# Kernel tuning notes

Measured on AMD Instinct MI355X. Metric: run time of the kernel, lower is better.

Reference implementation:

```python
import jax, jax.numpy as jnp
import numpy as np

D_MODEL = 96
D_STATE = 16
D_INNER = 192   # expand * d_model
DT_RANK = 6     # ceil(96/16)
D_DEPTH_OUT = 1024  # (64/2)*(64/2)
BATCH, HH, WW = 2, 64, 64


def silu(v):
    return v * jax.nn.sigmoid(v)


def setup_inputs() -> dict:
    key = jax.random.key(0)
    ks = jax.random.split(key, 10)
    f = jnp.float32
    x = jax.random.normal(ks[0], (BATCH, HH, WW, D_MODEL), f)
    in_proj_w = jax.random.normal(ks[1], (2 * D_INNER, D_MODEL), f) * 0.02
    conv2d_w = jax.random.normal(ks[2], (D_INNER, 1, 3, 3), f) * 0.1  # depthwise, groups=D_INNER
    conv2d_b = jnp.zeros((D_INNER,), f)
    depth_conv_w = jax.random.normal(ks[3], (D_INNER, 1, 3, 3), f) * 0.1  # depthwise, stride 2
    depth_conv_b = jnp.zeros((D_INNER,), f)
    depth_fc_w = jax.random.normal(ks[4], (D_INNER, D_DEPTH_OUT), f) * 0.02
    depth_fc_b = jnp.zeros((D_INNER,), f)
    x_proj_w = jax.random.normal(ks[5], (DT_RANK + 2 * D_STATE, D_INNER), f) * 0.02
    dt_init_std = DT_RANK ** (-0.5)
    dt_projs_w = jax.random.uniform(ks[6], (D_INNER, DT_RANK), f, -dt_init_std, dt_init_std)
    # inverse-softplus of dt ~ U(log 1e-3, log 0.1)
    dt = jnp.exp(jax.random.uniform(ks[7], (D_INNER,), f) * (np.log(0.1) - np.log(0.001)) + np.log(0.001))
    dt = jnp.clip(dt, 1e-4, None)
    dt_projs_b = dt + jnp.log(-jnp.expm1(-dt))
    A_logs = jnp.log(jnp.tile(jnp.arange(1, D_STATE + 1, dtype=f)[None, :], (D_INNER, 1)))
    Ds = jnp.ones((D_INNER,), f)
    out_norm_w = jnp.ones((D_INNER,), f)
    out_norm_b = jnp.zeros((D_INNER,), f)
    out_proj_w = jax.random.normal(ks[8], (D_MODEL, D_INNER), f) * 0.02
    return dict(x=x, in_proj_w=in_proj_w, conv2d_w=conv2d_w, conv2d_b=conv2d_b,
                depth_conv_w=depth_conv_w, depth_conv_b=depth_conv_b,
                depth_fc_w=depth_fc_w, depth_fc_b=depth_fc_b, x_proj_w=x_proj_w,
                dt_projs_w=dt_projs_w, dt_projs_b=dt_projs_b, A_logs=A_logs, Ds=Ds,
                out_norm_w=out_norm_w, out_norm_b=out_norm_b, out_proj_w=out_proj_w)


def _selective_scan(u, delta, A, Bm, Cm, D, delta_bias):
    # u, delta: [B, D, L]; A: [D, N]; Bm, Cm: [B, N, L]; D: [D]; delta_bias: [D]
    delta = jax.nn.softplus(delta + delta_bias[None, :, None])
    dA = jnp.exp(jnp.einsum('bdl,dn->lbdn', delta, A))          # [L,B,D,N]
    dBu = jnp.einsum('bdl,bnl,bdl->lbdn', delta, Bm, u)          # [L,B,D,N]
    Ct = jnp.transpose(Cm, (2, 0, 1))                            # [L,B,N]
    h0 = jnp.zeros(dA.shape[1:], u.dtype)

    def step(h, inp):
        a, b, c = inp
        h = a * h + b                                            # S6 recurrence
        return h, jnp.einsum('bdn,bn->bd', h, c)

    _, ys = jax.lax.scan(step, h0, (dA, dBu, Ct))                # ys: [L,B,D]
    y = jnp.transpose(ys, (1, 2, 0))                             # [B,D,L]
    return y + D[None, :, None] * u


def _forward(x, in_proj_w, conv2d_w, conv2d_b, depth_conv_w, depth_conv_b,
             depth_fc_w, depth_fc_b, x_proj_w, dt_projs_w, dt_projs_b,
             A_logs, Ds, out_norm_w, out_norm_b, out_proj_w):
    B, H, W, _ = x.shape
    Di, N, R = D_INNER, D_STATE, DT_RANK
    dn = ('NCHW', 'OIHW', 'NCHW')
    xz = x @ in_proj_w.T
    x1, z = jnp.split(xz, 2, axis=-1)
    xc = jnp.transpose(x1, (0, 3, 1, 2))                         # [B,Di,H,W]
    xc = jax.lax.conv_general_dilated(xc, conv2d_w, (1, 1), [(1, 1), (1, 1)],
                                      dimension_numbers=dn, feature_group_count=Di)
    xc = silu(xc + conv2d_b[None, :, None, None])
    dxc = jax.lax.conv_general_dilated(xc, depth_conv_w, (2, 2), [(1, 1), (1, 1)],
                                       dimension_numbers=dn, feature_group_count=Di)
    dxc = dxc + depth_conv_b[None, :, None, None]                # [B,Di,H/2,W/2]
    dx = dxc.reshape(B, Di, -1)                                  # [B,Di,1024]
    dx = dx @ depth_fc_w.T + depth_fc_b                          # [B,Di,Di]
    dx = silu(jnp.transpose(dx, (0, 2, 1)))                      # [B,Di,CC], CC=Di
    L = H * W
    CC = dx.shape[-1]
    xs = jnp.concatenate([dx, xc.reshape(B, Di, L)], axis=-1)    # mode='head': [B,Di,LL]
    x_dbl = jnp.einsum('bdl,cd->bcl', xs, x_proj_w)
    dts, Bm, Cm = x_dbl[:, :R], x_dbl[:, R:R + N], x_dbl[:, R + N:]
    dts = jnp.einsum('brl,dr->bdl', dts, dt_projs_w)
    A = -jnp.exp(A_logs)
    y = _selective_scan(xs, dts, A, Bm, Cm, Ds, dt_projs_b)
    y = y[..., CC:]                                              # drop depth tokens (head mode)
    y = jnp.transpose(y, (0, 2, 1)).reshape(B, H, W, Di)
    mu = jnp.mean(y, axis=-1, keepdims=True)
    var = jnp.var(y, axis=-1, keepdims=True)
    y = (y - mu) * jax.lax.rsqrt(var + 1e-5) * out_norm_w + out_norm_b
    y = y * silu(z)
    return y @ out_proj_w.T


def reference(x, in_proj_w, conv2d_w, conv2d_b, depth_conv_w, depth_conv_b,
              depth_fc_w, depth_fc_b, x_proj_w, dt_projs_w, dt_projs_b,
              A_logs, Ds, out_norm_w, out_norm_b, out_proj_w):
    return _forward(x, in_proj_w, conv2d_w, conv2d_b, depth_conv_w, depth_conv_b,
                    depth_fc_w, depth_fc_b, x_proj_w, dt_projs_w, dt_projs_b,
                    A_logs, Ds, out_norm_w, out_norm_b, out_proj_w)
```

## Files before the change

kernel.cpp:

```cpp
#include <hip/hip_runtime.h>
#include <hip/hip_bf16.h>

typedef __hip_bfloat16 bf16;

#define BATCH 2
#define DM 96
#define DI 192
#define LSP 4096
#define LD 192
#define LTOT 4288
#define NST 16
#define RK 6
#define DFC 1024
#define CLEN 64
#define NCH 67
#define SCH 64
#define XR 16
#define NG  (BATCH * DI * NST)

__device__ __forceinline__ float b2f(bf16 v) { return __bfloat162float(v); }
__device__ __forceinline__ float silu_f(float x) { return x / (1.f + __expf(-x)); }
__device__ __forceinline__ float softplus_f(float x) { return x > 20.f ? x : log1pf(__expf(x)); }

__device__ __forceinline__ int is_f32(const void* alog) {
    return ((const unsigned int*)alog)[0] == 0u;
}
__device__ __forceinline__ float LDI(const void* p, int i, int f32m) {
    return f32m ? ((const float*)p)[i] : __bfloat162float(((const bf16*)p)[i]);
}
__device__ __forceinline__ void unpack2(unsigned int u, float* o) {
    o[0] = __uint_as_float(u << 16);
    o[1] = __uint_as_float(u & 0xffff0000u);
}

__device__ __forceinline__ float row16_sum(float v) {
    v += __int_as_float(__builtin_amdgcn_update_dpp(0, __float_as_int(v), 0x128, 0xf, 0xf, true));
    v += __int_as_float(__builtin_amdgcn_update_dpp(0, __float_as_int(v), 0x124, 0xf, 0xf, true));
    v += __int_as_float(__builtin_amdgcn_update_dpp(0, __float_as_int(v), 0x122, 0xf, 0xf, true));
    v += __int_as_float(__builtin_amdgcn_update_dpp(0, __float_as_int(v), 0x121, 0xf, 0xf, true));
    return v;
}

#define TW(r, i)  ((r) * 64 + ((((i) >> 2) + (r)) & 15) * 4 + ((i) & 3))

__global__ __launch_bounds__(256) void k_wprep(const void* __restrict__ ipw, float* __restrict__ wT,
                                               const void* __restrict__ alog) {
    const int f32m = is_f32(alog);
    int idx = blockIdx.x * 256 + threadIdx.x;
    if (idx < 96 * 384) {
        int k = idx / 384, c = idx - k * 384;
        wT[idx] = LDI(ipw, c * 96 + k, f32m);
    }
}

__global__ __launch_bounds__(384) void k_inproj2(const void* __restrict__ x, const float* __restrict__ wT,
                                                 float* __restrict__ x1, float* __restrict__ z,
                                                 const void* __restrict__ alog) {
    __shared__ __align__(16) float sx[16 * 100];
    const int f32m = is_f32(alog);
    int t = threadIdx.x;
    int row0 = blockIdx.x * 16;
    {
        int e = t * 4;
        int row = e / 96, k = e - row * 96;
        float4 v;
        if (f32m) {
            v = *((const float4*)((const float*)x + (row0 + row) * 96 + k));
        } else {
            uint2 u = *((const uint2*)((const ushort*)x + (row0 + row) * 96 + k));
            float f[4];
            unpack2(u.x, &f[0]); unpack2(u.y, &f[2]);
            v = make_float4(f[0], f[1], f[2], f[3]);
        }
        *(float4*)&sx[row * 100 + k] = v;
    }
    __syncthreads();
    int rg = t / 96, cg = t - rg * 96;
    int c0 = cg * 4, rbase = rg * 4;
    float acc[4][4];
    #pragma unroll
    for (int r = 0; r < 4; r++)
        #pragma unroll
        for (int cc = 0; cc < 4; cc++) acc[r][cc] = 0.f;
    const float* wp = wT + c0;
    #pragma unroll 4
    for (int k4 = 0; k4 < 24; k4++) {
        float4 xv[4], wv[4];
        #pragma unroll
        for (int r = 0; r < 4; r++) xv[r] = *(const float4*)&sx[(rbase + r) * 100 + k4 * 4];
        #pragma unroll
        for (int q = 0; q < 4; q++) wv[q] = *(const float4*)&wp[(k4 * 4 + q) * 384];
        #pragma unroll
        for (int r = 0; r < 4; r++) {
            float xr[4] = {xv[r].x, xv[r].y, xv[r].z, xv[r].w};
            #pragma unroll
            for (int q = 0; q < 4; q++) {
                acc[r][0] += xr[q] * wv[q].x;
                acc[r][1] += xr[q] * wv[q].y;
                acc[r][2] += xr[q] * wv[q].z;
                acc[r][3] += xr[q] * wv[q].w;
            }
        }
    }
    #pragma unroll
    for (int r = 0; r < 4; r++) {
        int row = row0 + rbase + r;
        float4 o = make_float4(acc[r][0], acc[r][1], acc[r][2], acc[r][3]);
        if (c0 < DI) *(float4*)&x1[row * DI + c0] = o;
        else         *(float4*)&z[row * DI + (c0 - DI)] = o;
    }
}

__global__ __launch_bounds__(192) void k_conv1(const float* __restrict__ x1, const void* __restrict__ cw,
                                               const void* __restrict__ cb, float* __restrict__ xs,
                                               const void* __restrict__ alog) {
    const int f32m = is_f32(alog);
    int d = threadIdx.x;
    int blk = blockIdx.x;
    int b = blk >> 9;
    int rest = blk & 511;
    int h = rest >> 3, w0 = (rest & 7) * 8;
    float wgt[9];
    #pragma unroll
    for (int i = 0; i < 9; i++) wgt[i] = LDI(cw, d * 9 + i, f32m);
    float bias = LDI(cb, d, f32m);
    float val[3][10];
    #pragma unroll
    for (int dh = 0; dh < 3; dh++) {
        int hh = h + dh - 1;
        #pragma unroll
        for (int j = 0; j < 10; j++) {
            int ww = w0 + j - 1;
            val[dh][j] = ((unsigned)hh < 64u && (unsigned)ww < 64u)
                       ? x1[((b << 12) + (hh << 6) + ww) * DI + d] : 0.f;
        }
    }
    #pragma unroll
    for (int i = 0; i < 8; i++) {
        float acc = bias;
        #pragma unroll
        for (int dh = 0; dh < 3; dh++)
            #pragma unroll
            for (int dw = 0; dw < 3; dw++)
                acc += val[dh][i + dw] * wgt[dh * 3 + dw];
        xs[(b * LTOT + LD + (h << 6) + w0 + i) * DI + d] = silu_f(acc);
    }
}

__global__ __launch_bounds__(192) void k_conv2(const float* __restrict__ xs, const void* __restrict__ dw,
                                               const void* __restrict__ db, float* __restrict__ dxc,
                                               const void* __restrict__ alog) {
    const int f32m = is_f32(alog);
    int d = threadIdx.x;
    int blk = blockIdx.x;
    int b = blk >> 10, lp = blk & 1023;
    int hp = lp >> 5, wp = lp & 31;
    float acc = LDI(db, d, f32m);
    #pragma unroll
    for (int dh = 0; dh < 3; dh++) {
        int h = 2 * hp + dh - 1;
        if ((unsigned)h >= 64u) continue;
        #pragma unroll
        for (int dw_ = 0; dw_ < 3; dw_++) {
            int w_ = 2 * wp + dw_ - 1;
            if ((unsigned)w_ >= 64u) continue;
            acc += xs[(b * LTOT + LD + (h << 6) + w_) * DI + d] * LDI(dw, d * 9 + dh * 3 + dw_, f32m);
        }
    }
    dxc[(b * DFC + lp) * DI + d] = acc;
}

__global__ __launch_bounds__(192) void k_dfc(const float* __restrict__ dxc, const void* __restrict__ fw,
                                             float* __restrict__ part, const void* __restrict__ alog) {
    __shared__ float sfw[4 * 128];
    const int f32m = is_f32(alog);
    int t = threadIdx.x;
    int blk = blockIdx.x;
    int p = blk / 96;
    int rem = blk - p * 96;
    int b   = rem / 48;
    int ch0 = (rem % 48) * 4;
    int k0  = p * 128;
    for (int idx = t; idx < 4 * 128; idx += 192)
        sfw[idx] = LDI(fw, (ch0 + (idx >> 7)) * DFC + k0 + (idx & 127), f32m);
    __syncthreads();
    float a0 = 0.f, a1 = 0.f, a2 = 0.f, a3 = 0.f;
    #pragma unroll 8
    for (int k = 0; k < 128; k++) {
        float dv = dxc[(b * DFC + k0 + k) * DI + t];
        a0 += dv * sfw[k];
        a1 += dv * sfw[128 + k];
        a2 += dv * sfw[256 + k];
        a3 += dv * sfw[384 + k];
    }
    int ob = ((p * 2 + b) * 192 + t) * DI + ch0;
    *(float4*)&part[ob] = make_float4(a0, a1, a2, a3);
}

__global__ __launch_bounds__(256) void k_xdbl(const float* __restrict__ xs_r, float* __restrict__ xs_w,
                                              const float* __restrict__ part, const void* __restrict__ fb,
                                              const void* __restrict__ xpw,
                                              float* __restrict__ BCb, float* __restrict__ dts,
                                              const void* __restrict__ alog) {
    __shared__ float sw[38 * 196];
    __shared__ float srow[XR][196];
    const int f32m = is_f32(alog);
    int t = threadIdx.x;
    for (int c = t >> 3; c < 38; c += 32) {
        int seg = (t & 7) * 24;
        for (int k = seg; k < seg + 24; k++) sw[c * 196 + k] = LDI(xpw, c * DI + k, f32m);
    }
    int row0 = blockIdx.x * XR;
    int bb = row0 >= LTOT ? 1 : 0;
    int depth = (row0 - bb * LTOT) < LD;
    for (int idx = t; idx < XR * DI; idx += 256) {
        int row = idx / DI, k = idx - row * DI;
        int grow = row0 + row;
        float v;
        if (depth) {
            int tok = grow - bb * LTOT;
            int o = (bb * 192 + tok) * DI + k;
            v = 0.f;
            #pragma unroll
            for (int p = 0; p < 8; p++) v += part[o + p * 73728];
            v = silu_f(v + LDI(fb, k, f32m));
            xs_w[grow * DI + k] = v;
        } else {
            v = xs_r[grow * DI + k];
        }
        srow[row][k] = v;
    }
    __syncthreads();
    int r = t & 15, cg = t >> 4;
    float a0 = 0.f, a1 = 0.f, a2 = 0.f;
    const float4* w0 = (const float4*)&sw[cg * 196];
    const float4* w1 = (const float4*)&sw[(cg + 16) * 196];
    const float4* w2 = (const float4*)&sw[(cg < 6 ? cg + 32 : cg) * 196];
    const float4* xr = (const float4*)&srow[r][0];
    #pragma unroll 4
    for (int k = 0; k < 48; k++) {
        float4 xv = xr[k], v0 = w0[k], v1 = w1[k], v2 = w2[k];
        a0 += xv.x * v0.x + xv.y * v0.y + xv.z * v0.z + xv.w * v0.w;
        a1 += xv.x * v1.x + xv.y * v1.y + xv.z * v1.z + xv.w * v1.w;
        a2 += xv.x * v2.x + xv.y * v2.y + xv.z * v2.z + xv.w * v2.w;
    }
    int grow = row0 + r;
    if (cg < 6) dts[grow * 6 + cg] = a0;
    else        BCb[grow * 32 + (cg - 6)] = a0;
    BCb[grow * 32 + (cg + 10)] = a1;
    if (cg < 6) BCb[grow * 32 + (cg + 26)] = a2;
}

__device__ __forceinline__ void delta_block_T(const float* sdts, const float* sdwb, float* sdel, int t) {
    int e = t * 4;
    int i = e >> 4, dl = e & 15;
    #pragma unroll
    for (int q = 0; q < 4; q++) {
        int r = dl + q;
        float dv = sdwb[96 + r];
        #pragma unroll
        for (int r2 = 0; r2 < RK; r2++) dv += sdts[i * RK + r2] * sdwb[r * RK + r2];
        sdel[TW(r, i)] = softplus_f(dv);
    }
}

__global__ __launch_bounds__(256) void k_scan1(const float* __restrict__ dts, const float* __restrict__ xs,
                                               const float* __restrict__ BCb, const void* __restrict__ dtw,
                                               const void* __restrict__ dtb, const void* __restrict__ alog,
                                               float2* __restrict__ AH) {
    __shared__ __align__(16) float su[1024];
    __shared__ __align__(16) float sB[1024];
    __shared__ __align__(16) float sdel[1024];
    __shared__ float sdts[CLEN * RK];
    __shared__ float sdwb[112];
    const int f32m = is_f32(alog);
    int t = threadIdx.x;
    int beta = blockIdx.x;
    int b = beta / (12 * NCH);
    int rem = beta - b * (12 * NCH);
    int dblk = rem / NCH, ch = rem - dblk * NCH;
    int d0 = dblk * 16, l0 = ch * CLEN;
    int bL = b * LTOT;
    {
        int e = t * 4;
        int i = e >> 4, dd = e & 15;
        float4 uv = *(const float4*)&xs[(bL + l0 + i) * DI + d0 + dd];
        float4 bv = *(const float4*)&BCb[(bL + l0 + i) * 32 + dd];
        float uu[4] = {uv.x, uv.y, uv.z, uv.w};
        float vb[4] = {bv.x, bv.y, bv.z, bv.w};
        #pragma unroll
        for (int q = 0; q < 4; q++) {
            int w = TW(dd + q, i);
            su[w] = uu[q];
            sB[w] = vb[q];
        }
    }
    for (int idx = t; idx < CLEN * RK; idx += 256) sdts[idx] = dts[(bL + l0) * RK + idx];
    if (t < 96)            sdwb[t] = LDI(dtw, (d0 + t / 6) * RK + (t % 6), f32m);
    else if (t < 112)      sdwb[t] = LDI(dtb, d0 + (t - 96), f32m);
    __syncthreads();
    delta_block_T(sdts, sdwb, sdel, t);
    __syncthreads();
    int dloc = t >> 4, n = t & 15;
    int d = d0 + dloc;
    float A = -__expf(LDI(alog, d * NST + n, f32m));
    float h = 0.f, ap = 1.f;
    int bd = dloc * 64, bn = n * 64;
    #pragma unroll
    for (int i4 = 0; i4 < 16; i4++) {
        int od = bd + (((i4 + dloc) & 15) << 2);
        int on = bn + (((i4 + n) & 15) << 2);
        float de[4], uu[4], vb[4];
        *(float4*)de = *(const float4*)&sdel[od];
        *(float4*)uu = *(const float4*)&su[od];
        *(float4*)vb = *(const float4*)&sB[on];
        #pragma unroll
        for (int q = 0; q < 4; q++) {
            float a = __expf(de[q] * A);
            h = a * h + de[q] * vb[q] * uu[q];
            ap *= a;
        }
    }
    int g = ((b * DI + d) * NST) + n;
    AH[ch * NG + g] = make_float2(ap, h);
}

__global__ __launch_bounds__(64) void k_scan2(const float2* __restrict__ AH, float* __restrict__ He) {
    int g = blockIdx.x * 64 + threadIdx.x;
    float h = 0.f;
    for (int ch = 0; ch < NCH; ch++) {
        He[ch * NG + g] = h;
        float2 v = AH[ch * NG + g];
        h = v.x * h + v.y;
    }
}

__global__ __launch_bounds__(256) void k_scan3(const float* __restrict__ dts, const float* __restrict__ xs,
                                               const float* __restrict__ BCb, const void* __restrict__ dtw,
                                               const void* __restrict__ dtb, const void* __restrict__ alog,
                                               const void* __restrict__ Dsv, const float* __restrict__ He,
                                               float* __restrict__ y) {
    __shared__ __align__(16) float su[1024];
    __shared__ __align__(16) float sbc[2048];
    __shared__ __align__(16) float sdel[1024];
    __shared__ float sdts[CLEN * RK];
    __shared__ float sdwb[112];
    const int f32m = is_f32(alog);
    int t = threadIdx.x;
    int beta = blockIdx.x;
    int b = beta / (12 * SCH);
    int rem = beta - b * (12 * SCH);
    int dblk = rem / SCH, ch = (rem - dblk * SCH) + 3;
    int d0 = dblk * 16, l0 = ch * CLEN;
    int bL = b * LTOT;
    {
        int e = t * 4;
        int i = e >> 4, dd = e & 15;
        float4 uv = *(const float4*)&xs[(bL + l0 + i) * DI + d0 + dd];
        float uu[4] = {uv.x, uv.y, uv.z, uv.w};
        #pragma unroll
        for (int q = 0; q < 4; q++) su[TW(dd + q, i)] = uu[q];
    }
    #pragma unroll
    for (int q2 = 0; q2 < 2; q2++) {
        int e = (t + q2 * 256) * 4;
        int i = e >> 5, c = e & 31;
        float4 v = *(const float4*)&BCb[(bL + l0 + i) * 32 + c];
        float vv[4] = {v.x, v.y, v.z, v.w};
        #pragma unroll
        for (int q = 0; q < 4; q++) sbc[TW(c + q, i)] = vv[q];
    }
    for (int idx = t; idx < CLEN * RK; idx += 256) sdts[idx] = dts[(bL + l0) * RK + idx];
    if (t < 96)            sdwb[t] = LDI(dtw, (d0 + t / 6) * RK + (t % 6), f32m);
    else if (t < 112)      sdwb[t] = LDI(dtb, d0 + (t - 96), f32m);
    __syncthreads();
    delta_block_T(sdts, sdwb, sdel, t);
    __syncthreads();
    int dloc = t >> 4, n = t & 15;
    int d = d0 + dloc;
    float A = -__expf(LDI(alog, d * NST + n, f32m));
    float Dv = LDI(Dsv, d, f32m);
    int g = ((b * DI + d) * NST) + n;
    float h = He[ch * NG + g];
    int bd = dloc * 64, bn = n * 64;
    #pragma unroll
    for (int i4 = 0; i4 < 16; i4++) {
        int od = bd + (((i4 + dloc) & 15) << 2);
        int on = bn + (((i4 + n) & 15) << 2);
        float de[4], uu[4], vb[4], vc[4];
        *(float4*)de = *(const float4*)&sdel[od];
        *(float4*)uu = *(const float4*)&su[od];
        *(float4*)vb = *(const float4*)&sbc[on];
        *(float4*)vc = *(const float4*)&sbc[on + 1024];
        #pragma unroll
        for (int q = 0; q < 4; q++) {
            float a = __expf(de[q] * A);
            h = a * h + de[q] * vb[q] * uu[q];
            float yv = row16_sum(h * vc[q]);
            if (n == 0) {
                int l = l0 + i4 * 4 + q;
                y[(b * LSP + (l - LD)) * DI + d] = yv + Dv * uu[q];
            }
        }
    }
}

__global__ __launch_bounds__(384) void k_out(const float* __restrict__ y, const float* __restrict__ z,
                                             const void* __restrict__ nw, const void* __restrict__ nb,
                                             const void* __restrict__ opw, void* __restrict__ out,
                                             const void* __restrict__ alog) {
    __shared__ float sg[2][DI];
    __shared__ float sred[2][2][3];
    const int f32m = is_f32(alog);
    int t = threadIdx.x;
    int m = t >> 2, kh = t & 3;
    float wr[48];
    if (f32m) {
        const float4* wp = (const float4*)((const float*)opw + m * DI + kh * 48);
        #pragma unroll
        for (int i = 0; i < 12; i++) {
            float4 v = wp[i];
            wr[4*i] = v.x; wr[4*i+1] = v.y; wr[4*i+2] = v.z; wr[4*i+3] = v.w;
        }
    } else {
        const uint4* wp = (const uint4*)((const bf16*)opw + m * DI + kh * 48);
        #pragma unroll
        for (int i = 0; i < 6; i++) {
            uint4 v = wp[i];
            unpack2(v.x, &wr[8*i]);   unpack2(v.y, &wr[8*i+2]);
            unpack2(v.z, &wr[8*i+4]); unpack2(v.w, &wr[8*i+6]);
        }
    }
    float nwv = 0.f, nbv = 0.f;
    if (t < DI) { nwv = LDI(nw, t, f32m); nbv = LDI(nb, t, f32m); }
    int wv_ = t >> 6;
    int row0 = blockIdx.x * 16;
    for (int pr = 0; pr < 8; pr++) {
        int r0 = row0 + pr * 2, r1 = r0 + 1;
        float y0 = 0.f, z0 = 0.f, y1 = 0.f, z1 = 0.f;
        if (t < DI) {
            y0 = y[r0 * DI + t]; z0 = z[r0 * DI + t];
            y1 = y[r1 * DI + t]; z1 = z[r1 * DI + t];
            float s0 = y0, q0 = y0 * y0, s1 = y1, q1 = y1 * y1;
            #pragma unroll
            for (int off = 32; off; off >>= 1) {
                s0 += __shfl_xor(s0, off); q0 += __shfl_xor(q0, off);
                s1 += __shfl_xor(s1, off); q1 += __shfl_xor(q1, off);
            }
            if ((t & 63) == 0) {
                sred[0][0][wv_] = s0; sred[0][1][wv_] = q0;
                sred[1][0][wv_] = s1; sred[1][1][wv_] = q1;
            }
        }
        __syncthreads();
        if (t < DI) {
            float S0  = sred[0][0][0] + sred[0][0][1] + sred[0][0][2];
            float Q0  = sred[0][1][0] + sred[0][1][1] + sred[0][1][2];
            float S1  = sred[1][0][0] + sred[1][0][1] + sred[1][0][2];
            float Q1  = sred[1][1][0] + sred[1][1][1] + sred[1][1][2];
            float mu0 = S0 * (1.f / 192.f), var0 = Q0 * (1.f / 192.f) - mu0 * mu0;
            float mu1 = S1 * (1.f / 192.f), var1 = Q1 * (1.f / 192.f) - mu1 * mu1;
            float g0 = (y0 - mu0) * rsqrtf(var0 + 1e-5f) * nwv + nbv;
            g0 *= z0 / (1.f + __expf(-z0));
            float g1 = (y1 - mu1) * rsqrtf(var1 + 1e-5f) * nwv + nbv;
            g1 *= z1 / (1.f + __expf(-z1));
            sg[0][t] = g0;
            sg[1][t] = g1;
        }
        __syncthreads();
        const float* g0p = &sg[0][kh * 48];
        const float* g1p = &sg[1][kh * 48];
        float a0 = 0.f, a1 = 0.f;
        #pragma unroll
        for (int j = 0; j < 48; j++) {
            a0 += g0p[j] * wr[j];
            a1 += g1p[j] * wr[j];
        }
        a0 += __shfl_xor(a0, 1); a0 += __shfl_xor(a0, 2);
        a1 += __shfl_xor(a1, 1); a1 += __shfl_xor(a1, 2);
        if (kh == 0) {
            if (f32m) {
                ((float*)out)[r0 * DM + m] = a0;
                ((float*)out)[r1 * DM + m] = a1;
            } else {
                ((bf16*)out)[r0 * DM + m] = __float2bfloat16(a0);
                ((bf16*)out)[r1 * DM + m] = __float2bfloat16(a1);
            }
        }
    }
}

extern "C" void kernel_launch(void* const* d_in, const int* in_sizes, int n_in,
                              void* d_out, int out_size, void* d_ws, size_t ws_size,
                              hipStream_t stream) {
    (void)in_sizes; (void)n_in; (void)out_size; (void)ws_size;
    const void* x    = d_in[0];
    const void* ipw  = d_in[1];
    const void* c1w  = d_in[2];
    const void* c1b  = d_in[3];
    const void* c2w  = d_in[4];
    const void* c2b  = d_in[5];
    const void* fcw  = d_in[6];
    const void* fcb  = d_in[7];
    const void* xpw  = d_in[8];
    const void* dtw  = d_in[9];
    const void* dtb  = d_in[10];
    const void* alog = d_in[11];
    const void* Dsv  = d_in[12];
    const void* nw   = d_in[13];
    const void* nb   = d_in[14];
    const void* opw  = d_in[15];

    float* ws  = (float*)d_ws;
    float* x1  = ws;
    float* z   = x1  + BATCH * LSP * DI;
    float* xs  = z   + BATCH * LSP * DI;
    float* dxc = xs  + BATCH * LTOT * DI;
    float* BCb = dxc + BATCH * DFC * DI;
    float* dts = BCb + BATCH * LTOT * 32;
    float2* AH = (float2*)(dts + BATCH * LTOT * RK);
    float* He  = (float*)(AH + NCH * NG);
    float* wT  = He + NCH * NG;
    float* part = x1;
    float* y    = x1;

    k_wprep  <<<dim3(144), dim3(256), 0, stream>>>(ipw, wT, alog);
    k_inproj2<<<dim3(512), dim3(384), 0, stream>>>(x, wT, x1, z, alog);
    k_conv1  <<<dim3(1024), dim3(DI), 0, stream>>>(x1, c1w, c1b, xs, alog);
    k_conv2  <<<dim3(BATCH * DFC), dim3(DI), 0, stream>>>(xs, c2w, c2b, dxc, alog);
    k_dfc    <<<dim3(768), dim3(DI), 0, stream>>>(dxc, fcw, part, alog);
    k_xdbl   <<<dim3(536), dim3(256), 0, stream>>>(xs, xs, part, fcb, xpw, BCb, dts, alog);
    k_scan1  <<<dim3(BATCH * 12 * NCH), dim3(256), 0, stream>>>(dts, xs, BCb, dtw, dtb, alog, AH);
    k_scan2  <<<dim3(96), dim3(64), 0, stream>>>(AH, He);
    k_scan3  <<<dim3(BATCH * 12 * SCH), dim3(256), 0, stream>>>(dts, xs, BCb, dtw, dtb, alog, Dsv, He, y);
    k_out    <<<dim3(512), dim3(384), 0, stream>>>(y, z, nw, nb, opw, d_out, alog);
}
```

Measured before the change: 221.8 us.

## Fuse launches via atomic tickets and read in-proj weights directly

The weight-transpose prep kernel is removed. The input projection now keeps each output column's weights in registers, with two threads per column whose partial sums are combined by a lane shuffle. The stride-2 depth conv and the depth FC are merged into one kernel, and scan phase 1 and 2 into another. In each merged kernel, the last-arriving blocks (found with an atomic ticket counter) spin until every block has finished and then run the second stage. This cuts three launches and their gaps, but adds spin-waits whose progress depends on how blocks are scheduled, and it reduces parallelism in the tail stages.

```diff
diff --git a/kernel.cpp b/kernel.cpp
--- a/kernel.cpp
+++ b/kernel.cpp
@@ -17,8 +17,10 @@
 #define SCH 64
 #define XR 16
 #define NG  (BATCH * DI * NST)
-
-__device__ __forceinline__ float b2f(bf16 v) { return __bfloat162float(v); }
+#define CDFC_NB (BATCH * DFC)
+#define DFC_NB  768
+#define S1_NB   (BATCH * 12 * NCH)
+
 __device__ __forceinline__ float silu_f(float x) { return x / (1.f + __expf(-x)); }
 __device__ __forceinline__ float softplus_f(float x) { return x > 20.f ? x : log1pf(__expf(x)); }
 
@@ -43,71 +45,72 @@
 
 #define TW(r, i)  ((r) * 64 + ((((i) >> 2) + (r)) & 15) * 4 + ((i) & 3))
 
-__global__ __launch_bounds__(256) void k_wprep(const void* __restrict__ ipw, float* __restrict__ wT,
-                                               const void* __restrict__ alog) {
-    const int f32m = is_f32(alog);
-    int idx = blockIdx.x * 256 + threadIdx.x;
-    if (idx < 96 * 384) {
-        int k = idx / 384, c = idx - k * 384;
-        wT[idx] = LDI(ipw, c * 96 + k, f32m);
-    }
-}
-
-__global__ __launch_bounds__(384) void k_inproj2(const void* __restrict__ x, const float* __restrict__ wT,
-                                                 float* __restrict__ x1, float* __restrict__ z,
-                                                 const void* __restrict__ alog) {
-    __shared__ __align__(16) float sx[16 * 100];
+__global__ __launch_bounds__(768) void k_inproj(const void* __restrict__ x, const void* __restrict__ ipw,
+                                                const void* __restrict__ alog,
+                                                float* __restrict__ x1, float* __restrict__ z,
+                                                int* __restrict__ cnts) {
+    __shared__ uint4 sxr[384];
     const int f32m = is_f32(alog);
     int t = threadIdx.x;
+    if (blockIdx.x == 0 && t < 8) cnts[t] = 0;
+    int col = t >> 1;
+    int kh = t & 1;
     int row0 = blockIdx.x * 16;
-    {
-        int e = t * 4;
-        int row = e / 96, k = e - row * 96;
-        float4 v;
-        if (f32m) {
-            v = *((const float4*)((const float*)x + (row0 + row) * 96 + k));
-        } else {
-            uint2 u = *((const uint2*)((const ushort*)x + (row0 + row) * 96 + k));
-            float f[4];
-            unpack2(u.x, &f[0]); unpack2(u.y, &f[2]);
-            v = make_float4(f[0], f[1], f[2], f[3]);
-        }
-        *(float4*)&sx[row * 100 + k] = v;
-    }
-    __syncthreads();
-    int rg = t / 96, cg = t - rg * 96;
-    int c0 = cg * 4, rbase = rg * 4;
-    float acc[4][4];
-    #pragma unroll
-    for (int r = 0; r < 4; r++)
-        #pragma unroll
-        for (int cc = 0; cc < 4; cc++) acc[r][cc] = 0.f;
-    const float* wp = wT + c0;
-    #pragma unroll 4
-    for (int k4 = 0; k4 < 24; k4++) {
-        float4 xv[4], wv[4];
-        #pragma unroll
-        for (int r = 0; r < 4; r++) xv[r] = *(const float4*)&sx[(rbase + r) * 100 + k4 * 4];
-        #pragma unroll
-        for (int q = 0; q < 4; q++) wv[q] = *(const float4*)&wp[(k4 * 4 + q) * 384];
-        #pragma unroll
-        for (int r = 0; r < 4; r++) {
-            float xr[4] = {xv[r].x, xv[r].y, xv[r].z, xv[r].w};
+    float wr[48];
+    if (f32m) {
+        const float4* wp = (const float4*)((const float*)ipw + col * 96 + kh * 48);
+        #pragma unroll
+        for (int i = 0; i < 12; i++) {
+            float4 v = wp[i];
+            wr[4*i] = v.x; wr[4*i+1] = v.y; wr[4*i+2] = v.z; wr[4*i+3] = v.w;
+        }
+        if (t < 384) sxr[t] = ((const uint4*)((const float*)x + row0 * 96))[t];
+        __syncthreads();
+        for (int r = 0; r < 16; r++) {
+            const uint4* xr = &sxr[r * 24 + kh * 12];
+            float acc = 0.f;
             #pragma unroll
-            for (int q = 0; q < 4; q++) {
-                acc[r][0] += xr[q] * wv[q].x;
-                acc[r][1] += xr[q] * wv[q].y;
-                acc[r][2] += xr[q] * wv[q].z;
-                acc[r][3] += xr[q] * wv[q].w;
-            }
-        }
-    }
-    #pragma unroll
-    for (int r = 0; r < 4; r++) {
-        int row = row0 + rbase + r;
-        float4 o = make_float4(acc[r][0], acc[r][1], acc[r][2], acc[r][3]);
-        if (c0 < DI) *(float4*)&x1[row * DI + c0] = o;
-        else         *(float4*)&z[row * DI + (c0 - DI)] = o;
+            for (int i = 0; i < 12; i++) {
+                uint4 u = xr[i];
+                acc += __uint_as_float(u.x) * wr[4*i]   + __uint_as_float(u.y) * wr[4*i+1]
+                     + __uint_as_float(u.z) * wr[4*i+2] + __uint_as_float(u.w) * wr[4*i+3];
+            }
+            acc += __shfl_xor(acc, 1);
+            if (kh == 0) {
+                int row = row0 + r;
+                if (col < DI) x1[row * DI + col] = acc;
+                else          z[row * DI + (col - DI)] = acc;
+            }
+        }
+    } else {
+        const uint4* wp = (const uint4*)((const bf16*)ipw + col * 96 + kh * 48);
+        #pragma unroll
+        for (int i = 0; i < 6; i++) {
+            uint4 v = wp[i];
+            unpack2(v.x, &wr[8*i]);   unpack2(v.y, &wr[8*i+2]);
+            unpack2(v.z, &wr[8*i+4]); unpack2(v.w, &wr[8*i+6]);
+        }
+        if (t < 192) sxr[t] = ((const uint4*)((const bf16*)x + row0 * 96))[t];
+        __syncthreads();
+        for (int r = 0; r < 16; r++) {
+            const uint4* xr = &sxr[r * 12 + kh * 6];
+            float acc = 0.f;
+            #pragma unroll
+            for (int i = 0; i < 6; i++) {
+                uint4 xv = xr[i];
+                float xf8[8];
+                unpack2(xv.x, &xf8[0]); unpack2(xv.y, &xf8[2]);
+                unpack2(xv.z, &xf8[4]); unpack2(xv.w, &xf8[6]);
+                #pragma unroll
+                for (int j = 0; j < 8; j++) acc += xf8[j] * wr[8*i + j];
+            }
+            acc += __shfl_xor(acc, 1);
+            if (kh == 0) {
+                int row = row0 + r;
+                if (col < DI) x1[row * DI + col] = acc;
+                else          z[row * DI + (col - DI)] = acc;
+            }
+        }
     }
 }
 
@@ -147,37 +150,46 @@
     }
 }
 
-__global__ __launch_bounds__(192) void k_conv2(const float* __restrict__ xs, const void* __restrict__ dw,
-                                               const void* __restrict__ db, float* __restrict__ dxc,
-                                               const void* __restrict__ alog) {
-    const int f32m = is_f32(alog);
-    int d = threadIdx.x;
-    int blk = blockIdx.x;
-    int b = blk >> 10, lp = blk & 1023;
-    int hp = lp >> 5, wp = lp & 31;
-    float acc = LDI(db, d, f32m);
-    #pragma unroll
-    for (int dh = 0; dh < 3; dh++) {
-        int h = 2 * hp + dh - 1;
-        if ((unsigned)h >= 64u) continue;
-        #pragma unroll
-        for (int dw_ = 0; dw_ < 3; dw_++) {
-            int w_ = 2 * wp + dw_ - 1;
-            if ((unsigned)w_ >= 64u) continue;
-            acc += xs[(b * LTOT + LD + (h << 6) + w_) * DI + d] * LDI(dw, d * 9 + dh * 3 + dw_, f32m);
-        }
-    }
-    dxc[(b * DFC + lp) * DI + d] = acc;
-}
-
-__global__ __launch_bounds__(192) void k_dfc(const float* __restrict__ dxc, const void* __restrict__ fw,
-                                             float* __restrict__ part, const void* __restrict__ alog) {
+__global__ __launch_bounds__(192) void k_cdfc(const float* __restrict__ xs, const void* __restrict__ dw,
+                                              const void* __restrict__ db, float* __restrict__ dxc,
+                                              const void* __restrict__ fw, float* __restrict__ part,
+                                              const void* __restrict__ alog, int* __restrict__ done) {
     __shared__ float sfw[4 * 128];
+    __shared__ int stick;
     const int f32m = is_f32(alog);
     int t = threadIdx.x;
-    int blk = blockIdx.x;
-    int p = blk / 96;
-    int rem = blk - p * 96;
+    {
+        int blk = blockIdx.x;
+        int b = blk >> 10, lp = blk & 1023;
+        int hp = lp >> 5, wp = lp & 31;
+        float acc = LDI(db, t, f32m);
+        #pragma unroll
+        for (int dh = 0; dh < 3; dh++) {
+            int h = 2 * hp + dh - 1;
+            if ((unsigned)h >= 64u) continue;
+            #pragma unroll
+            for (int dw_ = 0; dw_ < 3; dw_++) {
+                int w_ = 2 * wp + dw_ - 1;
+                if ((unsigned)w_ >= 64u) continue;
+                acc += xs[(b * LTOT + LD + (h << 6) + w_) * DI + t] * LDI(dw, t * 9 + dh * 3 + dw_, f32m);
+            }
+        }
+        dxc[(b * DFC + lp) * DI + t] = acc;
+    }
+    __syncthreads();
+    if (t == 0) { __threadfence(); stick = atomicAdd(done, 1); }
+    __syncthreads();
+    int tick = stick;
+    if (tick < CDFC_NB - DFC_NB) return;
+    if (t == 0) {
+        while (__hip_atomic_load(done, __ATOMIC_ACQUIRE, __HIP_MEMORY_SCOPE_AGENT) < CDFC_NB)
+            __builtin_amdgcn_s_sleep(2);
+    }
+    __syncthreads();
+    __threadfence();
+    int slice = tick - (CDFC_NB - DFC_NB);
+    int p = slice / 96;
+    int rem = slice - p * 96;
     int b   = rem / 48;
     int ch0 = (rem % 48) * 4;
     int k0  = p * 128;
@@ -264,15 +276,17 @@
     }
 }
 
-__global__ __launch_bounds__(256) void k_scan1(const float* __restrict__ dts, const float* __restrict__ xs,
-                                               const float* __restrict__ BCb, const void* __restrict__ dtw,
-                                               const void* __restrict__ dtb, const void* __restrict__ alog,
-                                               float2* __restrict__ AH) {
+__global__ __launch_bounds__(256) void k_scan1m(const float* __restrict__ dts, const float* __restrict__ xs,
+                                                const float* __restrict__ BCb, const void* __restrict__ dtw,
+                                                const void* __restrict__ dtb, const void* __restrict__ alog,
+                                                float2* __restrict__ AH, float* __restrict__ He,
+                                                int* __restrict__ done) {
     __shared__ __align__(16) float su[1024];
     __shared__ __align__(16) float sB[1024];
     __shared__ __align__(16) float sdel[1024];
     __shared__ float sdts[CLEN * RK];
     __shared__ float sdwb[112];
+    __shared__ int stick;
     const int f32m = is_f32(alog);
     int t = threadIdx.x;
     int beta = blockIdx.x;
@@ -323,15 +337,26 @@
     }
     int g = ((b * DI + d) * NST) + n;
     AH[ch * NG + g] = make_float2(ap, h);
-}
-
-__global__ __launch_bounds__(64) void k_scan2(const float2* __restrict__ AH, float* __restrict__ He) {
-    int g = blockIdx.x * 64 + threadIdx.x;
-    float h = 0.f;
-    for (int ch = 0; ch < NCH; ch++) {
-        He[ch * NG + g] = h;
-        float2 v = AH[ch * NG + g];
-        h = v.x * h + v.y;
+    __syncthreads();
+    if (t == 0) { __threadfence(); stick = atomicAdd(done, 1); }
+    __syncthreads();
+    int tick = stick;
+    if (tick < S1_NB - 96) return;
+    if (t == 0) {
+        while (__hip_atomic_load(done, __ATOMIC_ACQUIRE, __HIP_MEMORY_SCOPE_AGENT) < S1_NB)
+            __builtin_amdgcn_s_sleep(2);
+    }
+    __syncthreads();
+    __threadfence();
+    int slice = tick - (S1_NB - 96);
+    if (t < 64) {
+        int g2 = slice * 64 + t;
+        float h2 = 0.f;
+        for (int c2 = 0; c2 < NCH; c2++) {
+            He[c2 * NG + g2] = h2;
+            float2 v = AH[c2 * NG + g2];
+            h2 = v.x * h2 + v.y;
+        }
     }
 }
 
@@ -520,18 +545,15 @@
     float* dts = BCb + BATCH * LTOT * 32;
     float2* AH = (float2*)(dts + BATCH * LTOT * RK);
     float* He  = (float*)(AH + NCH * NG);
-    float* wT  = He + NCH * NG;
+    int* cnts  = (int*)(He + NCH * NG);
     float* part = x1;
     float* y    = x1;
 
-    k_wprep  <<<dim3(144), dim3(256), 0, stream>>>(ipw, wT, alog);
-    k_inproj2<<<dim3(512), dim3(384), 0, stream>>>(x, wT, x1, z, alog);
-    k_conv1  <<<dim3(1024), dim3(DI), 0, stream>>>(x1, c1w, c1b, xs, alog);
-    k_conv2  <<<dim3(BATCH * DFC), dim3(DI), 0, stream>>>(xs, c2w, c2b, dxc, alog);
-    k_dfc    <<<dim3(768), dim3(DI), 0, stream>>>(dxc, fcw, part, alog);
-    k_xdbl   <<<dim3(536), dim3(256), 0, stream>>>(xs, xs, part, fcb, xpw, BCb, dts, alog);
-    k_scan1  <<<dim3(BATCH * 12 * NCH), dim3(256), 0, stream>>>(dts, xs, BCb, dtw, dtb, alog, AH);
-    k_scan2  <<<dim3(96), dim3(64), 0, stream>>>(AH, He);
-    k_scan3  <<<dim3(BATCH * 12 * SCH), dim3(256), 0, stream>>>(dts, xs, BCb, dtw, dtb, alog, Dsv, He, y);
-    k_out    <<<dim3(512), dim3(384), 0, stream>>>(y, z, nw, nb, opw, d_out, alog);
-}
+    k_inproj<<<dim3(512), dim3(768), 0, stream>>>(x, ipw, alog, x1, z, cnts);
+    k_conv1 <<<dim3(1024), dim3(DI), 0, stream>>>(x1, c1w, c1b, xs, alog);
+    k_cdfc  <<<dim3(CDFC_NB), dim3(DI), 0, stream>>>(xs, c2w, c2b, dxc, fcw, part, alog, &cnts[0]);
+    k_xdbl  <<<dim3(536), dim3(256), 0, stream>>>(xs, xs, part, fcb, xpw, BCb, dts, alog);
+    k_scan1m<<<dim3(S1_NB), dim3(256), 0, stream>>>(dts, xs, BCb, dtw, dtb, alog, AH, He, &cnts[1]);
+    k_scan3 <<<dim3(BATCH * 12 * SCH), dim3(256), 0, stream>>>(dts, xs, BCb, dtw, dtb, alog, Dsv, He, y);
+    k_out   <<<dim3(512), dim3(384), 0, stream>>>(y, z, nw, nb, opw, d_out, alog);
+}
```

New measurement: 389.7 us. 75.7% more time.

## Fuse stride-2 depthwise conv with depth FC into one kernel

Applied to the files above, without the earlier changes.

Replaces the separate stride-2 depthwise conv kernel and the split-K depth FC kernel with one fused kernel. Each block computes the conv output for 8 channels across all 1024 positions directly into shared memory, then runs the FC over the full reduction. This removes the dxc intermediate and the 8-way partial-sum buffer and its reduction in k_xdbl, and saves one launch. The trade-off is that only 48 blocks are launched, which leaves most CUs idle. Each block also re-reads the full FC weight matrix, and the strided conv loads per thread are uncoalesced across channels.

```diff
diff --git a/kernel.cpp b/kernel.cpp
--- a/kernel.cpp
+++ b/kernel.cpp
@@ -17,8 +17,8 @@
 #define SCH 64
 #define XR 16
 #define NG  (BATCH * DI * NST)
-
-__device__ __forceinline__ float b2f(bf16 v) { return __bfloat162float(v); }
+#define CD_CH 8
+
 __device__ __forceinline__ float silu_f(float x) { return x / (1.f + __expf(-x)); }
 __device__ __forceinline__ float softplus_f(float x) { return x > 20.f ? x : log1pf(__expf(x)); }
 
@@ -147,58 +147,82 @@
     }
 }
 
-__global__ __launch_bounds__(192) void k_conv2(const float* __restrict__ xs, const void* __restrict__ dw,
-                                               const void* __restrict__ db, float* __restrict__ dxc,
-                                               const void* __restrict__ alog) {
-    const int f32m = is_f32(alog);
-    int d = threadIdx.x;
-    int blk = blockIdx.x;
-    int b = blk >> 10, lp = blk & 1023;
-    int hp = lp >> 5, wp = lp & 31;
-    float acc = LDI(db, d, f32m);
-    #pragma unroll
-    for (int dh = 0; dh < 3; dh++) {
-        int h = 2 * hp + dh - 1;
-        if ((unsigned)h >= 64u) continue;
-        #pragma unroll
-        for (int dw_ = 0; dw_ < 3; dw_++) {
-            int w_ = 2 * wp + dw_ - 1;
-            if ((unsigned)w_ >= 64u) continue;
-            acc += xs[(b * LTOT + LD + (h << 6) + w_) * DI + d] * LDI(dw, d * 9 + dh * 3 + dw_, f32m);
-        }
-    }
-    dxc[(b * DFC + lp) * DI + d] = acc;
-}
-
-__global__ __launch_bounds__(192) void k_dfc(const float* __restrict__ dxc, const void* __restrict__ fw,
-                                             float* __restrict__ part, const void* __restrict__ alog) {
-    __shared__ float sfw[4 * 128];
+__global__ __launch_bounds__(384) void k_cdfc2(const float* __restrict__ xs, const void* __restrict__ dw,
+                                               const void* __restrict__ db, const void* __restrict__ fw,
+                                               float* __restrict__ dxf, const void* __restrict__ alog) {
+    __shared__ __align__(16) float dxcL[1024 * CD_CH];
+    __shared__ float sfwT[192 * 33];
+    __shared__ float sred[192 * CD_CH];
     const int f32m = is_f32(alog);
     int t = threadIdx.x;
-    int blk = blockIdx.x;
-    int p = blk / 96;
-    int rem = blk - p * 96;
-    int b   = rem / 48;
-    int ch0 = (rem % 48) * 4;
-    int k0  = p * 128;
-    for (int idx = t; idx < 4 * 128; idx += 192)
-        sfw[idx] = LDI(fw, (ch0 + (idx >> 7)) * DFC + k0 + (idx & 127), f32m);
-    __syncthreads();
-    float a0 = 0.f, a1 = 0.f, a2 = 0.f, a3 = 0.f;
-    #pragma unroll 8
-    for (int k = 0; k < 128; k++) {
-        float dv = dxc[(b * DFC + k0 + k) * DI + t];
-        a0 += dv * sfw[k];
-        a1 += dv * sfw[128 + k];
-        a2 += dv * sfw[256 + k];
-        a3 += dv * sfw[384 + k];
-    }
-    int ob = ((p * 2 + b) * 192 + t) * DI + ch0;
-    *(float4*)&part[ob] = make_float4(a0, a1, a2, a3);
+    int b  = blockIdx.x / 24;
+    int cg = blockIdx.x - b * 24;
+    int ch0 = cg * CD_CH;
+    for (int p2 = 0; p2 < 3; p2++) {
+        int pos = p2 * 384 + t;
+        if (pos < 1024) {
+            int hp = pos >> 5, wp = pos & 31;
+            #pragma unroll
+            for (int ch = 0; ch < CD_CH; ch++) {
+                int d = ch0 + ch;
+                float acc = LDI(db, d, f32m);
+                #pragma unroll
+                for (int dh = 0; dh < 3; dh++) {
+                    int h = 2 * hp + dh - 1;
+                    if ((unsigned)h >= 64u) continue;
+                    #pragma unroll
+                    for (int dw_ = 0; dw_ < 3; dw_++) {
+                        int w_ = 2 * wp + dw_ - 1;
+                        if ((unsigned)w_ >= 64u) continue;
+                        acc += xs[(b * LTOT + LD + (h << 6) + w_) * DI + d]
+                             * LDI(dw, d * 9 + dh * 3 + dw_, f32m);
+                    }
+                }
+                dxcL[pos * CD_CH + ch] = acc;
+            }
+        }
+    }
+    __syncthreads();
+    int jh = t / 192;
+    int c  = t - jh * 192;
+    float acc[CD_CH];
+    #pragma unroll
+    for (int i = 0; i < CD_CH; i++) acc[i] = 0.f;
+    for (int j0 = 0; j0 < DFC; j0 += 32) {
+        for (int e = t; e < 192 * 32; e += 384) {
+            int cc = e >> 5, jj = e & 31;
+            sfwT[cc * 33 + jj] = LDI(fw, cc * DFC + j0 + jj, f32m);
+        }
+        __syncthreads();
+        int jb = jh * 16;
+        #pragma unroll
+        for (int jj = 0; jj < 16; jj++) {
+            float w = sfwT[c * 33 + jb + jj];
+            const float* dp = &dxcL[(j0 + jb + jj) * CD_CH];
+            float d0[4], d1[4];
+            *(float4*)d0 = *(const float4*)dp;
+            *(float4*)d1 = *(const float4*)(dp + 4);
+            #pragma unroll
+            for (int i = 0; i < 4; i++) { acc[i] += d0[i] * w; acc[4 + i] += d1[i] * w; }
+        }
+        __syncthreads();
+    }
+    if (jh == 1) {
+        #pragma unroll
+        for (int i = 0; i < CD_CH; i++) sred[i * 192 + c] = acc[i];
+    }
+    __syncthreads();
+    if (jh == 0) {
+        #pragma unroll
+        for (int i = 0; i < CD_CH; i++) {
+            float v = acc[i] + sred[i * 192 + c];
+            dxf[(b * 192 + ch0 + i) * DI + c] = v;
+        }
+    }
 }
 
 __global__ __launch_bounds__(256) void k_xdbl(const float* __restrict__ xs_r, float* __restrict__ xs_w,
-                                              const float* __restrict__ part, const void* __restrict__ fb,
+                                              const float* __restrict__ dxf, const void* __restrict__ fb,
                                               const void* __restrict__ xpw,
                                               float* __restrict__ BCb, float* __restrict__ dts,
                                               const void* __restrict__ alog) {
@@ -219,11 +243,7 @@
         float v;
         if (depth) {
             int tok = grow - bb * LTOT;
-            int o = (bb * 192 + tok) * DI + k;
-            v = 0.f;
-            #pragma unroll
-            for (int p = 0; p < 8; p++) v += part[o + p * 73728];
-            v = silu_f(v + LDI(fb, k, f32m));
+            v = silu_f(dxf[(bb * 192 + tok) * DI + k] + LDI(fb, k, f32m));
             xs_w[grow * DI + k] = v;
         } else {
             v = xs_r[grow * DI + k];
@@ -521,15 +541,14 @@
     float2* AH = (float2*)(dts + BATCH * LTOT * RK);
     float* He  = (float*)(AH + NCH * NG);
     float* wT  = He + NCH * NG;
-    float* part = x1;
-    float* y    = x1;
+    float* dxf = x1;
+    float* y   = x1;
 
     k_wprep  <<<dim3(144), dim3(256), 0, stream>>>(ipw, wT, alog);
     k_inproj2<<<dim3(512), dim3(384), 0, stream>>>(x, wT, x1, z, alog);
     k_conv1  <<<dim3(1024), dim3(DI), 0, stream>>>(x1, c1w, c1b, xs, alog);
-    k_conv2  <<<dim3(BATCH * DFC), dim3(DI), 0, stream>>>(xs, c2w, c2b, dxc, alog);
-    k_dfc    <<<dim3(768), dim3(DI), 0, stream>>>(dxc, fcw, part, alog);
-    k_xdbl   <<<dim3(536), dim3(256), 0, stream>>>(xs, xs, part, fcb, xpw, BCb, dts, alog);
+    k_cdfc2  <<<dim3(BATCH * 24), dim3(384), 0, stream>>>(xs, c2w, c2b, fcw, dxf, alog);
+    k_xdbl   <<<dim3(536), dim3(256), 0, stream>>>(xs, xs, dxf, fcb, xpw, BCb, dts, alog);
     k_scan1  <<<dim3(BATCH * 12 * NCH), dim3(256), 0, stream>>>(dts, xs, BCb, dtw, dtb, alog, AH);
     k_scan2  <<<dim3(96), dim3(64), 0, stream>>>(AH, He);
     k_scan3  <<<dim3(BATCH * 12 * SCH), dim3(256), 0, stream>>>(dts, xs, BCb, dtw, dtb, alog, Dsv, He, y);
```

Measured after the change: 418.7 us. 88.8% more time.

## Fuse chunk-carry scan into scan1 via last-blocks atomic counter

Applied to the files above, without the earlier changes.

Removes the separate k_scan2 launch. Each scan1 block increments a global counter after writing its chunk summary. The last 96 blocks to finish spin until every block is done, then each runs one 64-thread carry propagation slice across chunks. The counter is reset in k_wprep. This saves one kernel launch and its gap, at the cost of spin-waiting, which relies on all earlier blocks making progress, and of a serial tail running on a few blocks.

```diff
diff --git a/kernel.cpp b/kernel.cpp
--- a/kernel.cpp
+++ b/kernel.cpp
@@ -17,8 +17,8 @@
 #define SCH 64
 #define XR 16
 #define NG  (BATCH * DI * NST)
-
-__device__ __forceinline__ float b2f(bf16 v) { return __bfloat162float(v); }
+#define S1_NB (BATCH * 12 * NCH)
+
 __device__ __forceinline__ float silu_f(float x) { return x / (1.f + __expf(-x)); }
 __device__ __forceinline__ float softplus_f(float x) { return x > 20.f ? x : log1pf(__expf(x)); }
 
@@ -44,9 +44,10 @@
 #define TW(r, i)  ((r) * 64 + ((((i) >> 2) + (r)) & 15) * 4 + ((i) & 3))
 
 __global__ __launch_bounds__(256) void k_wprep(const void* __restrict__ ipw, float* __restrict__ wT,
-                                               const void* __restrict__ alog) {
+                                               const void* __restrict__ alog, int* __restrict__ cnts) {
     const int f32m = is_f32(alog);
     int idx = blockIdx.x * 256 + threadIdx.x;
+    if (idx < 8) cnts[idx] = 0;
     if (idx < 96 * 384) {
         int k = idx / 384, c = idx - k * 384;
         wT[idx] = LDI(ipw, c * 96 + k, f32m);
@@ -264,15 +265,17 @@
     }
 }
 
-__global__ __launch_bounds__(256) void k_scan1(const float* __restrict__ dts, const float* __restrict__ xs,
-                                               const float* __restrict__ BCb, const void* __restrict__ dtw,
-                                               const void* __restrict__ dtb, const void* __restrict__ alog,
-                                               float2* __restrict__ AH) {
+__global__ __launch_bounds__(256) void k_scan1m(const float* __restrict__ dts, const float* __restrict__ xs,
+                                                const float* __restrict__ BCb, const void* __restrict__ dtw,
+                                                const void* __restrict__ dtb, const void* __restrict__ alog,
+                                                float2* __restrict__ AH, float* __restrict__ He,
+                                                int* __restrict__ done) {
     __shared__ __align__(16) float su[1024];
     __shared__ __align__(16) float sB[1024];
     __shared__ __align__(16) float sdel[1024];
     __shared__ float sdts[CLEN * RK];
     __shared__ float sdwb[112];
+    __shared__ int stick;
     const int f32m = is_f32(alog);
     int t = threadIdx.x;
     int beta = blockIdx.x;
@@ -323,15 +326,26 @@
     }
     int g = ((b * DI + d) * NST) + n;
     AH[ch * NG + g] = make_float2(ap, h);
-}
-
-__global__ __launch_bounds__(64) void k_scan2(const float2* __restrict__ AH, float* __restrict__ He) {
-    int g = blockIdx.x * 64 + threadIdx.x;
-    float h = 0.f;
-    for (int ch = 0; ch < NCH; ch++) {
-        He[ch * NG + g] = h;
-        float2 v = AH[ch * NG + g];
-        h = v.x * h + v.y;
+    __syncthreads();
+    if (t == 0) { __threadfence(); stick = atomicAdd(done, 1); }
+    __syncthreads();
+    int tick = stick;
+    if (tick < S1_NB - 96) return;
+    if (t == 0) {
+        while (__hip_atomic_load(done, __ATOMIC_ACQUIRE, __HIP_MEMORY_SCOPE_AGENT) < S1_NB)
+            __builtin_amdgcn_s_sleep(2);
+    }
+    __syncthreads();
+    __threadfence();
+    int slice = tick - (S1_NB - 96);
+    if (t < 64) {
+        int g2 = slice * 64 + t;
+        float h2 = 0.f;
+        for (int c2 = 0; c2 < NCH; c2++) {
+            He[c2 * NG + g2] = h2;
+            float2 v = AH[c2 * NG + g2];
+            h2 = v.x * h2 + v.y;
+        }
     }
 }
 
@@ -521,17 +535,17 @@
     float2* AH = (float2*)(dts + BATCH * LTOT * RK);
     float* He  = (float*)(AH + NCH * NG);
     float* wT  = He + NCH * NG;
+    int* cnts  = (int*)(wT + 96 * 384);
     float* part = x1;
     float* y    = x1;
 
-    k_wprep  <<<dim3(144), dim3(256), 0, stream>>>(ipw, wT, alog);
+    k_wprep  <<<dim3(144), dim3(256), 0, stream>>>(ipw, wT, alog, cnts);
     k_inproj2<<<dim3(512), dim3(384), 0, stream>>>(x, wT, x1, z, alog);
     k_conv1  <<<dim3(1024), dim3(DI), 0, stream>>>(x1, c1w, c1b, xs, alog);
     k_conv2  <<<dim3(BATCH * DFC), dim3(DI), 0, stream>>>(xs, c2w, c2b, dxc, alog);
     k_dfc    <<<dim3(768), dim3(DI), 0, stream>>>(dxc, fcw, part, alog);
     k_xdbl   <<<dim3(536), dim3(256), 0, stream>>>(xs, xs, part, fcb, xpw, BCb, dts, alog);
-    k_scan1  <<<dim3(BATCH * 12 * NCH), dim3(256), 0, stream>>>(dts, xs, BCb, dtw, dtb, alog, AH);
-    k_scan2  <<<dim3(96), dim3(64), 0, stream>>>(AH, He);
+    k_scan1m <<<dim3(S1_NB), dim3(256), 0, stream>>>(dts, xs, BCb, dtw, dtb, alog, AH, He, &cnts[0]);
     k_scan3  <<<dim3(BATCH * 12 * SCH), dim3(256), 0, stream>>>(dts, xs, BCb, dtw, dtb, alog, Dsv, He, y);
     k_out    <<<dim3(512), dim3(384), 0, stream>>>(y, z, nw, nb, opw, d_out, alog);
 }
```

Result: slower. 275.9 us (+24.4%).
